# Performance work log

Hardware: AMD Instinct MI355X
Metric: run time of the kernel (lower is better)

## Reference

```python
import jax, jax.numpy as jnp
import numpy as np

L_LEVELS = 16
N_FEATS = 2
BASE_RES = 16
LOG2_T = 19
T = 2 ** LOG2_T
BOUND = 1.0
DESIRED_RES = 2048 * BOUND
PER_LEVEL_SCALE = np.exp2(np.log2(DESIRED_RES / BASE_RES) / (L_LEVELS - 1))
PRIMES = np.array([1, 2654435761, 805459861], dtype=np.uint32)
# 8 trilinear corner offsets, [8,3]
OFFSETS = np.array([[(i >> d) & 1 for d in range(3)] for i in range(8)], dtype=np.uint32)


def hash_encode(x, table):
    """x: [N,3] in [-bound,bound]; table: [L, T, F]. Returns [N, L*F]."""
    x01 = jnp.clip((x + BOUND) / (2.0 * BOUND), 0.0, 1.0)  # [N,3]
    feats = []
    for l in range(L_LEVELS):
        scale = BASE_RES * (PER_LEVEL_SCALE ** l) - 1.0  # torch-ngp gridencoder convention
        res = int(np.ceil(scale)) + 1
        pos = x01 * jnp.float32(scale) + 0.5
        pg = jnp.floor(pos)
        frac = pos - pg                                   # [N,3]
        pgi = pg.astype(jnp.uint32)
        corners = pgi[:, None, :] + OFFSETS[None, :, :]   # [N,8,3] uint32
        if res ** 3 <= T:
            # grid small enough: direct (strided) indexing
            r = np.uint32(res)
            idx = corners[..., 0] + corners[..., 1] * r + corners[..., 2] * (r * r)
        else:
            # spatial hash (xor of coord*prime)
            idx = (corners[..., 0] * PRIMES[0]) ^ (corners[..., 1] * PRIMES[1]) ^ (corners[..., 2] * PRIMES[2])
        idx = (idx % np.uint32(T)).astype(jnp.int32)      # [N,8]
        f = table[l][idx]                                 # [N,8,F] gather
        # trilinear weights: prod over dims of frac (if corner bit=1) else 1-frac
        w = jnp.prod(jnp.where(OFFSETS[None, :, :] == 1, frac[:, None, :], 1.0 - frac[:, None, :]), axis=-1)  # [N,8]
        feats.append(jnp.sum(f * w[..., None], axis=1))   # [N,F]
    return jnp.concatenate(feats, axis=-1)                # [N, L*F]


def softplus_beta100(x):
    z = 100.0 * x
    return jnp.where(z > 20.0, x, jnp.log1p(jnp.exp(jnp.minimum(z, 20.0))) / 100.0)


def setup_inputs() -> dict:
    key = jax.random.key(0)
    k = jax.random.split(key, 6)
    N = 1048576
    in_dim = L_LEVELS * N_FEATS  # 32
    hidden = 64
    out_dim = 1 + 15             # sdf + geo_feat
    x = jax.random.uniform(k[0], (N, 3), jnp.float32, -1.0, 1.0)
    table = jax.random.uniform(k[1], (L_LEVELS, T, N_FEATS), jnp.float32, -1e-4, 1e-4)
    W0 = jax.random.normal(k[2], (hidden, in_dim), jnp.float32) * (1.0 / np.sqrt(in_dim))
    b0 = jnp.zeros((hidden,), jnp.float32)
    W1 = jax.random.normal(k[3], (out_dim, hidden), jnp.float32) * (1.0 / np.sqrt(hidden))
    b1 = jnp.zeros((out_dim,), jnp.float32)
    return {"x": x, "table": table, "W0": W0, "b0": b0, "W1": W1, "b1": b1}


def reference(x, table, W0, b0, W1, b1):
    enc = hash_encode(x, table)                      # [N,32]
    h = softplus_beta100(enc @ W0.T + b0)            # [N,64]
    h = h @ W1.T + b1                                # [N,16]
    sdf = h[..., :1]
    geo_feat = h[..., 1:]
    return (sdf, geo_feat)
```

## Files before the change

kernel.cpp:

```cpp
#include <hip/hip_runtime.h>
#include <math.h>

constexpr int      kLevels = 16;
constexpr unsigned kT      = 1u << 19;
constexpr int      kHidden = 64;
constexpr int      kInDim  = 32;
constexpr int      kOutDim = 16;

struct LevelParams {
    float    scale[kLevels];
    unsigned res[kLevels];
    unsigned dense[kLevels];
};

typedef __attribute__((ext_vector_type(8))) short bf16x8;
typedef __attribute__((ext_vector_type(4))) float f32x4;
typedef __attribute__((ext_vector_type(2))) unsigned uint2v;

__device__ inline float bf2f(unsigned short b) {
    unsigned u = ((unsigned)b) << 16;
    return __builtin_bit_cast(float, u);
}
__device__ inline unsigned short f2bf(float f) {
    unsigned u = __builtin_bit_cast(unsigned, f);
    unsigned r = (u + 0x7fffu + ((u >> 16) & 1u)) >> 16;
    return (unsigned short)r;
}
__device__ inline unsigned pack2bf(float a, float b) {
    return (unsigned)f2bf(a) | ((unsigned)f2bf(b) << 16);
}

__global__ __launch_bounds__(256) void convert_table(
        const float* __restrict__ t, unsigned* __restrict__ o, int n4)
{
    int i = blockIdx.x * blockDim.x + threadIdx.x;
    if (i >= n4) return;
    float4 v = ((const float4*)t)[i];
    ((uint2*)o)[i] = make_uint2(pack2bf(v.x, v.y), pack2bf(v.z, v.w));
}

__global__ __launch_bounds__(256) void encode_level(
        const float* __restrict__ x,
        const unsigned* __restrict__ tblAll,
        unsigned* __restrict__ enc,
        int N, int nxb, LevelParams lp)
{
    const int bid = blockIdx.x;
    const int tid = threadIdx.x;

    int l, xb;
    const int pinnedBlocks = 8 * nxb;
    if (bid < pinnedBlocks) {
        l  = 8 + (bid & 7);
        xb = bid >> 3;
    } else {
        const int r = bid - pinnedBlocks;
        l  = r / nxb;
        xb = r - l * nxb;
    }

    const float    scale = lp.scale[l];
    const unsigned res   = lp.res[l];
    const bool     dense = (lp.dense[l] != 0);
    const unsigned* tbl  = tblAll + (size_t)l * kT;

    const int pBase = xb * 1024 + tid;

    float xs[4], ys[4], zs[4];
    #pragma unroll
    for (int q = 0; q < 4; ++q) {
        int p = pBase + q * 256;
        if (p >= N) p = N - 1;
        xs[q] = x[3 * p + 0];
        ys[q] = x[3 * p + 1];
        zs[q] = x[3 * p + 2];
    }

    unsigned v0[4][4], v1[4][4];
    float    wyz[4][4], wgx[4], wfx[4];

    #pragma unroll
    for (int q = 0; q < 4; ++q) {
        const float x0 = fminf(fmaxf((xs[q] + 1.0f) * 0.5f, 0.0f), 1.0f);
        const float y0 = fminf(fmaxf((ys[q] + 1.0f) * 0.5f, 0.0f), 1.0f);
        const float z0 = fminf(fmaxf((zs[q] + 1.0f) * 0.5f, 0.0f), 1.0f);

        const float posx = x0 * scale + 0.5f;
        const float posy = y0 * scale + 0.5f;
        const float posz = z0 * scale + 0.5f;
        const float fgx = floorf(posx), fgy = floorf(posy), fgz = floorf(posz);
        const float fx = posx - fgx, fy = posy - fgy, fz = posz - fgz;
        const float gy = 1.0f - fy,  gz = 1.0f - fz;
        const unsigned ix = (unsigned)fgx, iy = (unsigned)fgy, iz = (unsigned)fgz;

        wgx[q] = 1.0f - fx;
        wfx[q] = fx;

        #pragma unroll
        for (int c2 = 0; c2 < 4; ++c2) {
            const unsigned cy = iy + (c2 & 1);
            const unsigned cz = iz + (c2 >> 1);
            wyz[q][c2] = ((c2 & 1) ? fy : gy) * ((c2 >> 1) ? fz : gz);

            if (dense) {
                const unsigned base = cy * res + cz * res * res;
                const unsigned idx0 = (ix + base) & (kT - 1u);
                if ((idx0 & 1u) == 0u) {
                    const uint2v pr = *(const uint2v*)(tbl + idx0);
                    v0[q][c2] = pr.x; v1[q][c2] = pr.y;
                } else {
                    v0[q][c2] = tbl[idx0];
                    v1[q][c2] = tbl[idx0 + 1u];
                }
            } else {
                const unsigned base = (cy * 2654435761u) ^ (cz * 805459861u);
                const unsigned idx0 = (ix ^ base) & (kT - 1u);
                if ((ix & 1u) == 0u) {
                    const unsigned b = idx0 & ~1u;
                    const uint2v pr = *(const uint2v*)(tbl + b);
                    const bool sw = (idx0 & 1u) != 0u;
                    v0[q][c2] = sw ? pr.y : pr.x;
                    v1[q][c2] = sw ? pr.x : pr.y;
                } else {
                    const unsigned idx1 = ((ix + 1u) ^ base) & (kT - 1u);
                    v0[q][c2] = tbl[idx0];
                    v1[q][c2] = tbl[idx1];
                }
            }
        }
    }

    #pragma unroll
    for (int q = 0; q < 4; ++q) {
        float a0 = 0.0f, a1 = 0.0f;
        #pragma unroll
        for (int c2 = 0; c2 < 4; ++c2) {
            const float w0 = wgx[q] * wyz[q][c2];
            const float w1 = wfx[q] * wyz[q][c2];
            a0 = fmaf(bf2f((unsigned short)(v0[q][c2] & 0xffffu)), w0, a0);
            a1 = fmaf(bf2f((unsigned short)(v0[q][c2] >> 16)),     w0, a1);
            a0 = fmaf(bf2f((unsigned short)(v1[q][c2] & 0xffffu)), w1, a0);
            a1 = fmaf(bf2f((unsigned short)(v1[q][c2] >> 16)),     w1, a1);
        }
        const int p = pBase + q * 256;
        if (p < N)
            __builtin_nontemporal_store(pack2bf(a0, a1), &enc[(size_t)l * N + p]);
    }
}

__global__ __launch_bounds__(256) void mlp_mfma(
        const unsigned* __restrict__ enc,
        const float* __restrict__ W0,
        const float* __restrict__ b0,
        const float* __restrict__ W1,
        const float* __restrict__ b1,
        float* __restrict__ out, int N, int nTiles)
{
    constexpr int kHStride = 72;
    __shared__ short lds_h[4][16 * kHStride];
    __shared__ float lds_o[4][16 * 16];

    const int wave = threadIdx.x >> 6;
    const int lane = threadIdx.x & 63;
    const int quad = lane >> 4;
    const int l16  = lane & 15;

    union Frag { bf16x8 v; short s[8]; unsigned u[4]; };

    Frag w0f[4];
    #pragma unroll
    for (int hb = 0; hb < 4; ++hb) {
        #pragma unroll
        for (int j = 0; j < 8; ++j) {
            const int k = quad * 8 + j;
            const int n = hb * 16 + l16;
            w0f[hb].s[j] = (short)f2bf(W0[n * kInDim + k]);
        }
    }
    Frag w1f[2];
    #pragma unroll
    for (int kb = 0; kb < 2; ++kb) {
        #pragma unroll
        for (int j = 0; j < 8; ++j) {
            const int k = kb * 32 + quad * 8 + j;
            const int n = l16;
            w1f[kb].s[j] = (short)f2bf(W1[n * kHidden + k]);
        }
    }
    float b0v[4];
    #pragma unroll
    for (int hb = 0; hb < 4; ++hb) b0v[hb] = b0[hb * 16 + l16];
    const float b1v = b1[l16];

    short* hrow = lds_h[wave];
    float* orow = lds_o[wave];
    const int waveGlobal = blockIdx.x * 4 + wave;
    const int nWaves     = gridDim.x * 4;

    auto loadFrag = [&](int t, Frag& f) {
        const int P = t * 16;
        int p = P + l16;
        if (p >= N) p = N - 1;
        #pragma unroll
        for (int j2 = 0; j2 < 4; ++j2)
            f.u[j2] = enc[(size_t)(quad * 4 + j2) * N + p];
    };

    int t = waveGlobal;
    if (t >= nTiles) return;

    Frag af;
    loadFrag(t, af);

    for (; t < nTiles; t += nWaves) {
        const int tn = t + nWaves;
        Frag afn;
        if (tn < nTiles) loadFrag(tn, afn);

        const int P = t * 16;

        f32x4 acc[4];
        #pragma unroll
        for (int hb = 0; hb < 4; ++hb) {
            acc[hb] = f32x4{b0v[hb], b0v[hb], b0v[hb], b0v[hb]};
            acc[hb] = __builtin_amdgcn_mfma_f32_16x16x32_bf16(
                          af.v, w0f[hb].v, acc[hb], 0, 0, 0);
        }

        #pragma unroll
        for (int hb = 0; hb < 4; ++hb) {
            #pragma unroll
            for (int r = 0; r < 4; ++r) {
                const float a = acc[hb][r];
                const float z = 100.0f * a;
                const float h = (z > 20.0f) ? a
                              : (__logf(1.0f + __expf(z)) * 0.01f);
                const int row = quad * 4 + r;
                const int col = hb * 16 + l16;
                hrow[row * kHStride + col] = (short)f2bf(h);
            }
        }
        bf16x8 h0 = *(const bf16x8*)&hrow[l16 * kHStride + quad * 8];
        bf16x8 h1 = *(const bf16x8*)&hrow[l16 * kHStride + 32 + quad * 8];

        f32x4 acc2 = f32x4{b1v, b1v, b1v, b1v};
        acc2 = __builtin_amdgcn_mfma_f32_16x16x32_bf16(h0, w1f[0].v, acc2, 0, 0, 0);
        acc2 = __builtin_amdgcn_mfma_f32_16x16x32_bf16(h1, w1f[1].v, acc2, 0, 0, 0);

        #pragma unroll
        for (int r = 0; r < 4; ++r)
            orow[(quad * 4 + r) * 16 + l16] = acc2[r];

        float* gbase = out + (size_t)N + (size_t)P * 15u;
        #pragma unroll
        for (int gp = 0; gp < 4; ++gp) {
            const int g = gp * 64 + lane;
            if (g < 240) {
                const int pt = g / 15;
                const int k  = g - pt * 15;
                if (P + pt < N)
                    __builtin_nontemporal_store(orow[pt * 16 + k + 1], &gbase[g]);
            }
        }
        if (lane < 16 && P + lane < N)
            __builtin_nontemporal_store(orow[lane * 16 + 0], &out[P + lane]);

        af = afn;
    }
}

__global__ __launch_bounds__(256) void sdf_fused(
        const float* __restrict__ x, const float* __restrict__ table,
        const float* __restrict__ W0, const float* __restrict__ b0,
        const float* __restrict__ W1, const float* __restrict__ b1,
        float* __restrict__ out, int N, LevelParams lp)
{
    const int gid = blockIdx.x * blockDim.x + threadIdx.x;
    if (gid >= N) return;
    const float x0 = fminf(fmaxf((x[3 * gid + 0] + 1.0f) * 0.5f, 0.0f), 1.0f);
    const float y0 = fminf(fmaxf((x[3 * gid + 1] + 1.0f) * 0.5f, 0.0f), 1.0f);
    const float z0 = fminf(fmaxf((x[3 * gid + 2] + 1.0f) * 0.5f, 0.0f), 1.0f);
    float enc[kInDim];
    #pragma unroll
    for (int l = 0; l < kLevels; ++l) {
        const float scale = lp.scale[l];
        const unsigned res = lp.res[l];
        const bool dense = (lp.dense[l] != 0);
        const float posx = x0 * scale + 0.5f, posy = y0 * scale + 0.5f, posz = z0 * scale + 0.5f;
        const float fgx = floorf(posx), fgy = floorf(posy), fgz = floorf(posz);
        const float fx = posx - fgx, fy = posy - fgy, fz = posz - fgz;
        const float gx = 1.0f - fx, gy = 1.0f - fy, gz = 1.0f - fz;
        const unsigned ix = (unsigned)fgx, iy = (unsigned)fgy, iz = (unsigned)fgz;
        const float* tbl = table + (size_t)l * kT * 2u;
        float a0 = 0.0f, a1 = 0.0f;
        #pragma unroll
        for (int c = 0; c < 8; ++c) {
            const unsigned cx = ix + (c & 1), cy = iy + ((c >> 1) & 1), cz = iz + ((c >> 2) & 1);
            unsigned idx = dense ? (cx + cy * res + cz * res * res)
                                 : (cx ^ (cy * 2654435761u) ^ (cz * 805459861u));
            idx &= (kT - 1u);
            const float2 tv = *(const float2*)(tbl + 2u * idx);
            const float w = ((c & 1) ? fx : gx) * (((c >> 1) & 1) ? fy : gy) * (((c >> 2) & 1) ? fz : gz);
            a0 = fmaf(tv.x, w, a0); a1 = fmaf(tv.y, w, a1);
        }
        enc[2 * l] = a0; enc[2 * l + 1] = a1;
    }
    float acc[kOutDim];
    #pragma unroll
    for (int k = 0; k < kOutDim; ++k) acc[k] = b1[k];
    #pragma unroll 2
    for (int j = 0; j < kHidden; ++j) {
        float a = b0[j];
        #pragma unroll
        for (int i = 0; i < kInDim; ++i) a = fmaf(enc[i], W0[j * kInDim + i], a);
        const float z = 100.0f * a;
        const float h = (z > 20.0f) ? a : (__logf(1.0f + __expf(z)) * 0.01f);
        #pragma unroll
        for (int k = 0; k < kOutDim; ++k) acc[k] = fmaf(h, W1[k * kHidden + j], acc[k]);
    }
    out[gid] = acc[0];
    #pragma unroll
    for (int k = 0; k < 15; ++k) out[(size_t)N + (size_t)gid * 15u + k] = acc[k + 1];
}

extern "C" void kernel_launch(void* const* d_in, const int* in_sizes, int n_in,
                              void* d_out, int out_size, void* d_ws, size_t ws_size,
                              hipStream_t stream) {
    const float* x     = (const float*)d_in[0];
    const float* table = (const float*)d_in[1];
    const float* W0    = (const float*)d_in[2];
    const float* b0    = (const float*)d_in[3];
    const float* W1    = (const float*)d_in[4];
    const float* b1    = (const float*)d_in[5];
    float* out = (float*)d_out;
    const int N = in_sizes[0] / 3;

    LevelParams lp;
    const double s = exp2(7.0 / 15.0);
    for (int l = 0; l < kLevels; ++l) {
        const double sc = 16.0 * pow(s, (double)l) - 1.0;
        lp.scale[l] = (float)sc;
        const unsigned res = (unsigned)ceil(sc) + 1u;
        lp.res[l] = res;
        lp.dense[l] =
            ((unsigned long long)res * res * res <= (unsigned long long)kT) ? 1u : 0u;
    }

    const size_t tbl_bytes = (size_t)kLevels * kT * 4u;
    const size_t enc_bytes = (size_t)kLevels * (size_t)N * 4u;

    if (ws_size >= tbl_bytes + enc_bytes) {
        unsigned* tbl_bf = (unsigned*)d_ws;
        unsigned* enc    = (unsigned*)((char*)d_ws + tbl_bytes);

        const int n4 = (int)(kLevels * kT * 2u / 4u);
        hipLaunchKernelGGL(convert_table, dim3((n4 + 255) / 256), dim3(256), 0, stream,
                           table, tbl_bf, n4);

        const int nxb = (N + 1023) / 1024;
        hipLaunchKernelGGL(encode_level, dim3(16 * nxb), dim3(256), 0, stream,
                           x, tbl_bf, enc, N, nxb, lp);

        const int nTiles = (N + 15) / 16;
        hipLaunchKernelGGL(mlp_mfma, dim3(2048), dim3(256), 0, stream,
                           enc, W0, b0, W1, b1, out, N, nTiles);
    } else {
        hipLaunchKernelGGL(sdf_fused, dim3((N + 255) / 256), dim3(256), 0, stream,
                           x, table, W0, b0, W1, b1, out, N, lp);
    }
}
```

Before: 435.6 us.

## Pipeline encode and MLP across point chunks in combined stage kernels

Merges the encode and MLP kernels into one stage kernel and splits the points into four chunks. Each launch encodes chunk i while running the MLP on chunk i-1, so the gather-bound encode overlaps the MFMA work. MLP loads of the encoded features become nontemporal loads. The cost is five launches instead of two, a smaller MLP grid of 512 blocks, and encode blocks now competing with MLP blocks for the same compute units.

```diff
diff --git a/kernel.cpp b/kernel.cpp
--- a/kernel.cpp
+++ b/kernel.cpp
@@ -39,15 +39,13 @@
     ((uint2*)o)[i] = make_uint2(pack2bf(v.x, v.y), pack2bf(v.z, v.w));
 }
 
-__global__ __launch_bounds__(256) void encode_level(
+__device__ __forceinline__ void encode_body(
         const float* __restrict__ x,
         const unsigned* __restrict__ tblAll,
         unsigned* __restrict__ enc,
-        int N, int nxb, LevelParams lp)
-{
-    const int bid = blockIdx.x;
-    const int tid = threadIdx.x;
-
+        int N, int nxb, int chunkStart, const LevelParams& lp,
+        int bid, int tid)
+{
     int l, xb;
     const int pinnedBlocks = 8 * nxb;
     if (bid < pinnedBlocks) {
@@ -64,7 +62,7 @@
     const bool     dense = (lp.dense[l] != 0);
     const unsigned* tbl  = tblAll + (size_t)l * kT;
 
-    const int pBase = xb * 1024 + tid;
+    const int pBase = chunkStart + xb * 1024 + tid;
 
     float xs[4], ys[4], zs[4];
     #pragma unroll
@@ -148,13 +146,12 @@
     }
 }
 
-__global__ __launch_bounds__(256) void mlp_mfma(
+__device__ __forceinline__ void mlp_body(
         const unsigned* __restrict__ enc,
-        const float* __restrict__ W0,
-        const float* __restrict__ b0,
-        const float* __restrict__ W1,
-        const float* __restrict__ b1,
-        float* __restrict__ out, int N, int nTiles)
+        const float* __restrict__ W0, const float* __restrict__ b0,
+        const float* __restrict__ W1, const float* __restrict__ b1,
+        float* __restrict__ out, int N, int tStart, int tEnd,
+        int mbid, int nMlpWaves)
 {
     constexpr int kHStride = 72;
     __shared__ short lds_h[4][16 * kHStride];
@@ -194,8 +191,6 @@
 
     short* hrow = lds_h[wave];
     float* orow = lds_o[wave];
-    const int waveGlobal = blockIdx.x * 4 + wave;
-    const int nWaves     = gridDim.x * 4;
 
     auto loadFrag = [&](int t, Frag& f) {
         const int P = t * 16;
@@ -203,19 +198,20 @@
         if (p >= N) p = N - 1;
         #pragma unroll
         for (int j2 = 0; j2 < 4; ++j2)
-            f.u[j2] = enc[(size_t)(quad * 4 + j2) * N + p];
+            f.u[j2] = __builtin_nontemporal_load(
+                          &enc[(size_t)(quad * 4 + j2) * N + p]);
     };
 
-    int t = waveGlobal;
-    if (t >= nTiles) return;
+    int t = tStart + mbid * 4 + wave;
+    if (t >= tEnd) return;
 
     Frag af;
     loadFrag(t, af);
 
-    for (; t < nTiles; t += nWaves) {
-        const int tn = t + nWaves;
+    for (; t < tEnd; t += nMlpWaves) {
+        const int tn = t + nMlpWaves;
         Frag afn;
-        if (tn < nTiles) loadFrag(tn, afn);
+        if (tn < tEnd) loadFrag(tn, afn);
 
         const int P = t * 16;
 
@@ -269,6 +265,29 @@
     }
 }
 
+__global__ __launch_bounds__(256) void stage_kernel(
+        const float* __restrict__ x,
+        const unsigned* __restrict__ tblAll,
+        unsigned* __restrict__ enc,
+        const float* __restrict__ W0, const float* __restrict__ b0,
+        const float* __restrict__ W1, const float* __restrict__ b1,
+        float* __restrict__ out,
+        int N, int nxbC, int chunkPts, int ce, int cm,
+        int encBlocks, int nTiles, LevelParams lp)
+{
+    if ((int)blockIdx.x < encBlocks) {
+        encode_body(x, tblAll, enc, N, nxbC, ce * chunkPts, lp,
+                    blockIdx.x, threadIdx.x);
+    } else {
+        const int mbid = blockIdx.x - encBlocks;
+        const int nMlpWaves = (gridDim.x - encBlocks) * 4;
+        const int tpc = chunkPts / 16;
+        const int tStart = cm * tpc;
+        const int tEnd = min(tStart + tpc, nTiles);
+        mlp_body(enc, W0, b0, W1, b1, out, N, tStart, tEnd, mbid, nMlpWaves);
+    }
+}
+
 __global__ __launch_bounds__(256) void sdf_fused(
         const float* __restrict__ x, const float* __restrict__ table,
         const float* __restrict__ W0, const float* __restrict__ b0,
@@ -357,13 +376,22 @@
         hipLaunchKernelGGL(convert_table, dim3((n4 + 255) / 256), dim3(256), 0, stream,
                            table, tbl_bf, n4);
 
-        const int nxb = (N + 1023) / 1024;
-        hipLaunchKernelGGL(encode_level, dim3(16 * nxb), dim3(256), 0, stream,
-                           x, tbl_bf, enc, N, nxb, lp);
-
+        constexpr int NCHUNK = 4;
+        const int chunkPts = (((N + NCHUNK - 1) / NCHUNK) + 1023) & ~1023;
+        const int nxbC = chunkPts / 1024;
+        const int encB = 16 * nxbC;
+        const int mlpB = 512;
         const int nTiles = (N + 15) / 16;
-        hipLaunchKernelGGL(mlp_mfma, dim3(2048), dim3(256), 0, stream,
-                           enc, W0, b0, W1, b1, out, N, nTiles);
+
+        for (int st = 0; st <= NCHUNK; ++st) {
+            const int ce = (st < NCHUNK) ? st : -1;
+            const int cm = st - 1;
+            const int eb = (ce >= 0) ? encB : 0;
+            const int mb = (cm >= 0) ? mlpB : 0;
+            hipLaunchKernelGGL(stage_kernel, dim3(eb + mb), dim3(256), 0, stream,
+                               x, tbl_bf, enc, W0, b0, W1, b1, out,
+                               N, nxbC, chunkPts, ce, cm, eb, nTiles, lp);
+        }
     } else {
         hipLaunchKernelGGL(sdf_fused, dim3((N + 255) / 256), dim3(256), 0, stream,
                            x, table, W0, b0, W1, b1, out, N, lp);
```

After: 514.8 us. 18.2% more time.
